# Kernel tuning notes

Hardware: AMD Instinct MI355X
Metric: run time of the kernel (lower is better)

## Reference

```python
import jax, jax.numpy as jnp
import numpy as np

B = 32
D_MODEL = 512
D_INNER = 2048
N_HEAD = 8
D_K = 64
D_V = 64


def layer_norm(x, g, b, eps=1e-5):
    m = jnp.mean(x, axis=-1, keepdims=True)
    v = jnp.mean((x - m) ** 2, axis=-1, keepdims=True)
    return (x - m) / jnp.sqrt(v + eps) * g + b


def _build_ragged():
    rs = np.random.RandomState(0)
    num_objs = rs.randint(120, 161, size=B)
    num_edges = rs.randint(480, 641, size=B)
    Lq = int(num_objs.max())
    Lv = int(num_edges.max())
    # non_pad_mask: True for valid query (entity) slots
    non_pad = np.arange(Lq)[None, :] < num_objs[:, None]  # (B, Lq)
    # slf_attn_mask semantics: True = masked out (-inf).
    # start all True, un-mask padded query rows (they get zeroed later anyway),
    # then un-mask (entity, edge) positions for each relation pair.
    mask = np.ones((B, Lq, Lv), dtype=bool)
    mask &= non_pad[:, :, None]  # pad query rows -> all False (unmasked)
    for i in range(B):
        ne, no = int(num_edges[i]), int(num_objs[i])
        j = np.arange(ne)
        subj = j % no              # guarantees every entity has >=1 edge
        obj = (j * 7 + 3) % no
        mask[i, subj, j] = False
        mask[i, obj, j] = False
    gather_idx = np.nonzero(non_pad.reshape(-1))[0].astype(np.int32)
    return Lq, Lv, non_pad, mask, gather_idx


def setup_inputs() -> dict:
    key = jax.random.key(0)
    ks = jax.random.split(key, 12)
    Lq, Lv, non_pad, mask, gather_idx = _build_ragged()
    s = 0.02
    f32 = jnp.float32
    return {
        "entity_feat": jax.random.normal(ks[0], (B, Lq, D_MODEL), f32),
        "predicate_feat": jax.random.normal(ks[1], (B, Lv, D_MODEL), f32),
        "w_qs": s * jax.random.normal(ks[2], (N_HEAD * D_K, D_MODEL), f32),
        "b_qs": jnp.zeros((N_HEAD * D_K,), f32),
        "w_ks": s * jax.random.normal(ks[3], (N_HEAD * D_K, D_MODEL), f32),
        "b_ks": jnp.zeros((N_HEAD * D_K,), f32),
        "w_vs": s * jax.random.normal(ks[4], (N_HEAD * D_V, D_MODEL), f32),
        "b_vs": jnp.zeros((N_HEAD * D_V,), f32),
        "w_fc": s * jax.random.normal(ks[5], (D_MODEL, N_HEAD * D_V), f32),
        "b_fc": jnp.zeros((D_MODEL,), f32),
        "ln1_g": jnp.ones((D_MODEL,), f32),
        "ln1_b": jnp.zeros((D_MODEL,), f32),
        "w1": s * jax.random.normal(ks[6], (D_INNER, D_MODEL), f32),
        "b1": jnp.zeros((D_INNER,), f32),
        "w2": s * jax.random.normal(ks[7], (D_MODEL, D_INNER), f32),
        "b2": jnp.zeros((D_MODEL,), f32),
        "ln2_g": jnp.ones((D_MODEL,), f32),
        "ln2_b": jnp.zeros((D_MODEL,), f32),
        "attn_mask": jnp.asarray(mask),
        "non_pad_mask": jnp.asarray(non_pad),
        "gather_idx": jnp.asarray(gather_idx),
    }


def reference(entity_feat, predicate_feat, w_qs, b_qs, w_ks, b_ks, w_vs, b_vs,
              w_fc, b_fc, ln1_g, ln1_b, w1, b1, w2, b2, ln2_g, ln2_b,
              attn_mask, non_pad_mask, gather_idx):
    Bsz, Lq, D = entity_feat.shape
    Lv = predicate_feat.shape[1]
    # multi-head cross attention: entities (queries) attend to predicates (kv)
    q = (entity_feat @ w_qs.T + b_qs).reshape(Bsz, Lq, N_HEAD, D_K)
    k = (predicate_feat @ w_ks.T + b_ks).reshape(Bsz, Lv, N_HEAD, D_K)
    v = (predicate_feat @ w_vs.T + b_vs).reshape(Bsz, Lv, N_HEAD, D_V)
    scores = jnp.einsum('bqhd,bkhd->bhqk', q, k) / jnp.sqrt(jnp.float32(D_K))
    scores = jnp.where(attn_mask[:, None, :, :], -jnp.inf, scores)
    attn = jax.nn.softmax(scores, axis=-1)
    ctx = jnp.einsum('bhqk,bkhd->bqhd', attn, v).reshape(Bsz, Lq, N_HEAD * D_V)
    out = ctx @ w_fc.T + b_fc
    out = layer_norm(out + entity_feat, ln1_g, ln1_b)
    npm = non_pad_mask[:, :, None].astype(out.dtype)
    out = out * npm
    # position-wise FFN (two 1x1 convs == linears) with residual + LayerNorm
    h = jax.nn.relu(out @ w1.T + b1)
    f = h @ w2.T + b2
    f = layer_norm(f + out, ln2_g, ln2_b)
    f = f * npm
    # unpad: gather valid entity rows
    return jnp.take(f.reshape(Bsz * Lq, D), gather_idx, axis=0)
```

## Files before the change

kernel.cpp:

```cpp
#include <hip/hip_runtime.h>
#include <math.h>

#define B_  32
#define H_  8
#define DM_ 512
#define DI_ 2048

typedef unsigned short u16;
typedef short s16x8 __attribute__((ext_vector_type(8)));
typedef short s16x4 __attribute__((ext_vector_type(4)));
typedef float f32x4 __attribute__((ext_vector_type(4)));

__device__ __forceinline__ float b2f(u16 u) {
  return __uint_as_float(((unsigned)u) << 16);
}
__device__ __forceinline__ u16 f2b(float f) {
  unsigned u = __float_as_uint(f);
  return (u16)((u + 0x7fffu + ((u >> 16) & 1u)) >> 16);
}

template<int ADT, int EPI, int RDT, int OUTF>
__global__ __launch_bounds__(256)
void gemm_mfma(const void* __restrict__ Av, const float* __restrict__ W,
               const float* __restrict__ bias, const void* __restrict__ Rv,
               void* __restrict__ Cout, int M, int N, int K)
{
  __shared__ u16 As[128 * 72];
  __shared__ u16 Bs[128 * 72];
  const int t = threadIdx.x;
  const int bm = blockIdx.y * 128, bn = blockIdx.x * 128;
  const int lane = t & 63, wave = t >> 6;
  const int lr = lane & 15, kg = lane >> 4;
  const int wr = wave >> 1, wc = wave & 1;
  const int srow = t >> 3, schk = (t & 7) * 8;

  f32x4 acc[4][4] = {};

  for (int k0 = 0; k0 < K; k0 += 64) {
#pragma unroll
    for (int p = 0; p < 4; p++) {
      const int r = srow + p * 32;
      s16x8 av = {};
      if (bm + r < M) {
        if (ADT == 0) {
          const float* ap = (const float*)Av + (size_t)(bm + r) * K + k0 + schk;
          const float4 a0 = *(const float4*)ap;
          const float4 a1 = *(const float4*)(ap + 4);
          av[0] = (short)f2b(a0.x); av[1] = (short)f2b(a0.y);
          av[2] = (short)f2b(a0.z); av[3] = (short)f2b(a0.w);
          av[4] = (short)f2b(a1.x); av[5] = (short)f2b(a1.y);
          av[6] = (short)f2b(a1.z); av[7] = (short)f2b(a1.w);
        } else {
          av = *(const s16x8*)((const u16*)Av + (size_t)(bm + r) * K + k0 + schk);
        }
      }
      *(s16x8*)&As[r * 72 + schk] = av;
      const float* wp = W + (size_t)(bn + r) * K + k0 + schk;
      const float4 w0 = *(const float4*)wp;
      const float4 w1 = *(const float4*)(wp + 4);
      s16x8 wv;
      wv[0] = (short)f2b(w0.x); wv[1] = (short)f2b(w0.y);
      wv[2] = (short)f2b(w0.z); wv[3] = (short)f2b(w0.w);
      wv[4] = (short)f2b(w1.x); wv[5] = (short)f2b(w1.y);
      wv[6] = (short)f2b(w1.z); wv[7] = (short)f2b(w1.w);
      *(s16x8*)&Bs[r * 72 + schk] = wv;
    }
    __syncthreads();
#pragma unroll
    for (int ks = 0; ks < 2; ks++) {
      s16x8 af[4], bg[4];
#pragma unroll
      for (int m = 0; m < 4; m++)
        af[m] = *(const s16x8*)&As[(wr * 64 + m * 16 + lr) * 72 + ks * 32 + kg * 8];
#pragma unroll
      for (int n = 0; n < 4; n++)
        bg[n] = *(const s16x8*)&Bs[(wc * 64 + n * 16 + lr) * 72 + ks * 32 + kg * 8];
#pragma unroll
      for (int m = 0; m < 4; m++)
#pragma unroll
        for (int n = 0; n < 4; n++)
          acc[m][n] = __builtin_amdgcn_mfma_f32_16x16x32_bf16(af[m], bg[n], acc[m][n], 0, 0, 0);
    }
    __syncthreads();
  }

  float bv[4];
#pragma unroll
  for (int n = 0; n < 4; n++) bv[n] = bias[bn + wc * 64 + n * 16 + lr];
#pragma unroll
  for (int m = 0; m < 4; m++) {
#pragma unroll
    for (int j = 0; j < 4; j++) {
      const int row = bm + wr * 64 + m * 16 + kg * 4 + j;
      if (row >= M) continue;
#pragma unroll
      for (int n = 0; n < 4; n++) {
        const int col = bn + wc * 64 + n * 16 + lr;
        float x = acc[m][n][j] + bv[n];
        if (EPI == 1) x = fmaxf(x, 0.f);
        if (EPI == 2) {
          if (RDT == 0) x += ((const float*)Rv)[(size_t)row * N + col];
          else          x += b2f(((const u16*)Rv)[(size_t)row * N + col]);
        }
        if (OUTF) ((u16*)Cout)[(size_t)row * N + col] = f2b(x);
        else      ((float*)Cout)[(size_t)row * N + col] = x;
      }
    }
  }
}

__global__ __launch_bounds__(256)
void transpose_k(const u16* __restrict__ X, u16* __restrict__ Y, int Lv, int Lvp)
{
  __shared__ u16 s[32][34];
  const int b = blockIdx.z, n0 = blockIdx.y * 32, j0 = blockIdx.x * 32;
  const int tx = threadIdx.x & 31, ty = threadIdx.x >> 5;
#pragma unroll
  for (int yy = 0; yy < 4; yy++) {
    const int j = j0 + ty + yy * 8;
    s[ty + yy * 8][tx] = (j < Lv) ? X[((size_t)b * Lv + j) * DM_ + n0 + tx] : (u16)0;
  }
  __syncthreads();
  const int j = j0 + tx;
#pragma unroll
  for (int yy = 0; yy < 4; yy++) {
    const int n = n0 + ty + yy * 8;
    Y[((size_t)b * DM_ + n) * Lvp + j] = s[tx][ty + yy * 8];
  }
}

__global__ __launch_bounds__(256)
void attn_mfma(const u16* __restrict__ Q, const u16* __restrict__ K,
               const u16* __restrict__ Vt, const int* __restrict__ mask,
               u16* __restrict__ ctxb, int Lq, int Lv, int Lvp)
{
  __shared__ u16 Ks[64][72];
  __shared__ u16 Vts[64][72];
  __shared__ u16 Plds[4][16][72];
  const float SENT = -1e30f;
  const int qb = blockIdx.x, h = blockIdx.y, b = blockIdx.z;
  const int t = threadIdx.x, w = t >> 6, lane = t & 63;
  const int lr = lane & 15, g = lane >> 4;
  const int q0 = qb * 64 + w * 16;
  const int myq = min(q0 + lr, Lq - 1);

  s16x8 qf[2];
  const u16* qptr = Q + ((size_t)b * Lq + myq) * DM_ + h * 64;
#pragma unroll
  for (int ks = 0; ks < 2; ks++) qf[ks] = *(const s16x8*)(qptr + ks * 32 + g * 8);

  const int* mrow = mask + ((size_t)b * Lq + myq) * (size_t)Lv;

  f32x4 Ot[4] = {};
  float mx = SENT, l = 0.f;

  const int srow = t >> 2, sc16 = (t & 3) * 16;
  const u16* kbase  = K + (size_t)b * Lv * DM_ + h * 64;
  const u16* vtbase = Vt + ((size_t)b * DM_ + h * 64) * (size_t)Lvp;

  for (int j0 = 0; j0 < Lv; j0 += 64) {
    __syncthreads();
    {
      const int j = j0 + srow;
      if (j < Lv) {
        const u16* kp = kbase + (size_t)j * DM_ + sc16;
        *(s16x8*)&Ks[srow][sc16]     = *(const s16x8*)kp;
        *(s16x8*)&Ks[srow][sc16 + 8] = *(const s16x8*)(kp + 8);
      } else {
        const s16x8 z = {};
        *(s16x8*)&Ks[srow][sc16] = z; *(s16x8*)&Ks[srow][sc16 + 8] = z;
      }
      const u16* vp = vtbase + (size_t)srow * Lvp + j0 + sc16;
      *(s16x8*)&Vts[srow][sc16]     = *(const s16x8*)vp;
      *(s16x8*)&Vts[srow][sc16 + 8] = *(const s16x8*)(vp + 8);
    }
    __syncthreads();

    f32x4 Sa[4] = {};
#pragma unroll
    for (int ks = 0; ks < 2; ks++) {
#pragma unroll
      for (int m = 0; m < 4; m++) {
        const s16x8 kf = *(const s16x8*)&Ks[m * 16 + lr][ks * 32 + g * 8];
        Sa[m] = __builtin_amdgcn_mfma_f32_16x16x32_bf16(kf, qf[ks], Sa[m], 0, 0, 0);
      }
    }

    float sv[4][4];
    float pm = SENT;
#pragma unroll
    for (int m = 0; m < 4; m++)
#pragma unroll
      for (int r = 0; r < 4; r++) {
        const int j = j0 + m * 16 + g * 4 + r;
        const int jc = min(j, Lv - 1);
        float x = Sa[m][r] * 0.125f;
        x = ((j >= Lv) || (mrow[jc] != 0)) ? SENT : x;
        sv[m][r] = x;
        pm = fmaxf(pm, x);
      }
    pm = fmaxf(pm, __shfl_xor(pm, 16));
    pm = fmaxf(pm, __shfl_xor(pm, 32));
    float pr[4][4];
    if (pm > -1e29f) {
      const float mn = fmaxf(mx, pm);
      const float scale = __expf(mx - mn);
      float ls = 0.f;
#pragma unroll
      for (int m = 0; m < 4; m++)
#pragma unroll
        for (int r = 0; r < 4; r++) {
          const float p = __expf(sv[m][r] - mn);
          pr[m][r] = p; ls += p;
        }
      ls += __shfl_xor(ls, 16);
      ls += __shfl_xor(ls, 32);
      l = l * scale + ls;
      mx = mn;
#pragma unroll
      for (int m = 0; m < 4; m++) Ot[m] *= scale;
    } else {
#pragma unroll
      for (int m = 0; m < 4; m++)
#pragma unroll
        for (int r = 0; r < 4; r++) pr[m][r] = 0.f;
    }

#pragma unroll
    for (int m = 0; m < 4; m++) {
      const unsigned lo = (unsigned)f2b(pr[m][0]) | ((unsigned)f2b(pr[m][1]) << 16);
      const unsigned hi = (unsigned)f2b(pr[m][2]) | ((unsigned)f2b(pr[m][3]) << 16);
      *(uint2*)&Plds[w][lr][m * 16 + g * 4] = make_uint2(lo, hi);
    }
    __syncthreads();

#pragma unroll
    for (int ks = 0; ks < 2; ks++) {
#pragma unroll
      for (int m = 0; m < 4; m++) {
        const s16x8 vf = *(const s16x8*)&Vts[m * 16 + lr][ks * 32 + g * 8];
        const s16x8 pf = *(const s16x8*)&Plds[w][lr][ks * 32 + g * 8];
        Ot[m] = __builtin_amdgcn_mfma_f32_16x16x32_bf16(vf, pf, Ot[m], 0, 0, 0);
      }
    }
  }

  __syncthreads();
  const float inv = l > 0.f ? 1.f / l : 0.f;
#pragma unroll
  for (int m = 0; m < 4; m++) {
    const unsigned lo = (unsigned)f2b(Ot[m][0] * inv) | ((unsigned)f2b(Ot[m][1] * inv) << 16);
    const unsigned hi = (unsigned)f2b(Ot[m][2] * inv) | ((unsigned)f2b(Ot[m][3] * inv) << 16);
    *(uint2*)&Plds[w][lr][m * 16 + g * 4] = make_uint2(lo, hi);
  }
  __syncthreads();
  const int oq = lane >> 2, od = (lane & 3) * 16;
  if (q0 + oq < Lq) {
    u16* op = ctxb + ((size_t)b * Lq + q0 + oq) * DM_ + h * 64 + od;
    *(s16x8*)op       = *(const s16x8*)&Plds[w][oq][od];
    *(s16x8*)(op + 8) = *(const s16x8*)&Plds[w][oq][od + 8];
  }
}

template<int OUTF>
__global__ __launch_bounds__(256)
void ln_mask_kernel(const float* __restrict__ X, const float* __restrict__ g,
                    const float* __restrict__ bta, const int* __restrict__ npm,
                    void* __restrict__ Y)
{
  __shared__ float sm[8];
  const int row = blockIdx.x;
  const int t = threadIdx.x;
  const float2 x = *(const float2*)&X[(size_t)row * DM_ + t * 2];

  float s = x.x + x.y;
#pragma unroll
  for (int o = 32; o; o >>= 1) s += __shfl_xor(s, o);
  if ((t & 63) == 0) sm[t >> 6] = s;
  __syncthreads();
  const float mean = (sm[0] + sm[1] + sm[2] + sm[3]) * (1.f / DM_);

  const float d0 = x.x - mean, d1 = x.y - mean;
  float vs = d0 * d0 + d1 * d1;
#pragma unroll
  for (int o = 32; o; o >>= 1) vs += __shfl_xor(vs, o);
  if ((t & 63) == 0) sm[4 + (t >> 6)] = vs;
  __syncthreads();
  const float var = (sm[4] + sm[5] + sm[6] + sm[7]) * (1.f / DM_);

  const float inv = rsqrtf(var + 1e-5f);
  const float np = npm[row] ? 1.f : 0.f;
  const int c = t * 2;
  const float y0 = (d0 * inv * g[c]     + bta[c])     * np;
  const float y1 = (d1 * inv * g[c + 1] + bta[c + 1]) * np;
  if (OUTF) {
    const unsigned pair = (unsigned)f2b(y0) | ((unsigned)f2b(y1) << 16);
    *(unsigned*)((u16*)Y + (size_t)row * DM_ + c) = pair;
  } else {
    *(float2*)((float*)Y + (size_t)row * DM_ + c) = make_float2(y0, y1);
  }
}

__global__ __launch_bounds__(128)
void gather_kernel(const float* __restrict__ F, const int* __restrict__ idx,
                   float* __restrict__ out)
{
  const int i = blockIdx.x;
  const int t = threadIdx.x;
  const int r = idx[i];
  *(float4*)&out[(size_t)i * DM_ + t * 4] =
      *(const float4*)&F[(size_t)r * DM_ + t * 4];
}

extern "C" void kernel_launch(void* const* d_in, const int* in_sizes, int n_in,
                              void* d_out, int out_size, void* d_ws, size_t ws_size,
                              hipStream_t stream)
{
  const float* entity = (const float*)d_in[0];
  const float* pred   = (const float*)d_in[1];
  const float* w_qs = (const float*)d_in[2];
  const float* b_qs = (const float*)d_in[3];
  const float* w_ks = (const float*)d_in[4];
  const float* b_ks = (const float*)d_in[5];
  const float* w_vs = (const float*)d_in[6];
  const float* b_vs = (const float*)d_in[7];
  const float* w_fc = (const float*)d_in[8];
  const float* b_fc = (const float*)d_in[9];
  const float* ln1g = (const float*)d_in[10];
  const float* ln1b = (const float*)d_in[11];
  const float* w1   = (const float*)d_in[12];
  const float* b1   = (const float*)d_in[13];
  const float* w2   = (const float*)d_in[14];
  const float* b2   = (const float*)d_in[15];
  const float* ln2g = (const float*)d_in[16];
  const float* ln2b = (const float*)d_in[17];
  const int* amask = (const int*)d_in[18];
  const int* npm   = (const int*)d_in[19];
  const int* gidx  = (const int*)d_in[20];

  const int Lq = in_sizes[0] / (B_ * DM_);
  const int Lv = in_sizes[1] / (B_ * DM_);
  const int Lvp = (Lv + 63) & ~63;
  const int nValid = in_sizes[20];
  const int Mq = B_ * Lq, Mv = B_ * Lv;

  auto algn = [](size_t x) { return (x + 255) & ~(size_t)255; };
  const size_t bKV  = (size_t)Mv * DM_ * 2;
  const size_t bVT  = (size_t)B_ * DM_ * Lvp * 2;
  const size_t bTMP = (size_t)Mq * DM_ * 4;
  const size_t bH   = (size_t)Mq * DI_ * 2;
  const size_t bQ   = (size_t)Mq * DM_ * 2;
  const size_t szR1 = algn(bKV > bTMP ? bKV : bTMP);
  const size_t szR2 = algn(bKV > bH ? bKV : bH);
  const size_t szR3 = algn(bQ);
  const size_t szR4 = algn(bQ);
  const size_t szR5 = algn(bVT);
  if (szR1 + szR2 + szR3 + szR4 + szR5 > ws_size) return;

  char* base = (char*)d_ws;
  char* R1 = base;
  char* R2 = R1 + szR1;
  char* R3 = R2 + szR2;
  char* R4 = R3 + szR3;
  char* R5 = R4 + szR4;

  u16*   Kb   = (u16*)R1;  float* tmp1 = (float*)R1;
  float* tmp2 = (float*)R1; float* ffin = (float*)R1;
  u16*   Vb   = (u16*)R2;  u16* hb = (u16*)R2;
  u16*   Qb   = (u16*)R3;  u16* out1 = (u16*)R3;
  u16*   ctxb = (u16*)R4;
  u16*   Vtb  = (u16*)R5;

  const dim3 blk(256);
  gemm_mfma<0, 0, 0, 1><<<dim3(DM_ / 128, (Mq + 127) / 128), blk, 0, stream>>>(
      entity, w_qs, b_qs, nullptr, Qb, Mq, DM_, DM_);
  gemm_mfma<0, 0, 0, 1><<<dim3(DM_ / 128, (Mv + 127) / 128), blk, 0, stream>>>(
      pred, w_ks, b_ks, nullptr, Kb, Mv, DM_, DM_);
  gemm_mfma<0, 0, 0, 1><<<dim3(DM_ / 128, (Mv + 127) / 128), blk, 0, stream>>>(
      pred, w_vs, b_vs, nullptr, Vb, Mv, DM_, DM_);
  transpose_k<<<dim3(Lvp / 32, DM_ / 32, B_), blk, 0, stream>>>(Vb, Vtb, Lv, Lvp);
  attn_mfma<<<dim3((Lq + 63) / 64, H_, B_), blk, 0, stream>>>(
      Qb, Kb, Vtb, amask, ctxb, Lq, Lv, Lvp);
  gemm_mfma<1, 2, 0, 0><<<dim3(DM_ / 128, (Mq + 127) / 128), blk, 0, stream>>>(
      ctxb, w_fc, b_fc, entity, tmp1, Mq, DM_, DM_);
  ln_mask_kernel<1><<<dim3(Mq), blk, 0, stream>>>(tmp1, ln1g, ln1b, npm, out1);
  gemm_mfma<1, 1, 0, 1><<<dim3(DI_ / 128, (Mq + 127) / 128), blk, 0, stream>>>(
      out1, w1, b1, nullptr, hb, Mq, DI_, DM_);
  gemm_mfma<1, 2, 1, 0><<<dim3(DM_ / 128, (Mq + 127) / 128), blk, 0, stream>>>(
      hb, w2, b2, out1, tmp2, Mq, DM_, DI_);
  ln_mask_kernel<0><<<dim3(Mq), blk, 0, stream>>>(tmp2, ln2g, ln2b, npm, ffin);
  gather_kernel<<<dim3(nValid), dim3(128), 0, stream>>>(ffin, gidx, (float*)d_out);
}
```

Before: 512.9 us.

## Pre-convert inputs and weights to bf16 and fuse K/V projections

Adds a single batched conversion kernel that turns the entity and predicate activations and all weight matrices into bf16 before any GEMM runs, so the GEMMs load bf16 directly instead of converting fp32 in every tile load. The K and V projections are merged into one GEMM with N=1024 that writes an interleaved KV buffer, using a split bias. The V transpose and the attention kernel now read from that interleaved layout. This removes repeated fp32 loads and conversion work per tile, especially for weights that many blocks re-read, at the cost of an extra conversion pass and a reorganised workspace layout.

```diff
diff --git a/kernel.cpp b/kernel.cpp
--- a/kernel.cpp
+++ b/kernel.cpp
@@ -8,7 +8,6 @@
 
 typedef unsigned short u16;
 typedef short s16x8 __attribute__((ext_vector_type(8)));
-typedef short s16x4 __attribute__((ext_vector_type(4)));
 typedef float f32x4 __attribute__((ext_vector_type(4)));
 
 __device__ __forceinline__ float b2f(u16 u) {
@@ -19,11 +18,35 @@
   return (u16)((u + 0x7fffu + ((u >> 16) & 1u)) >> 16);
 }
 
-template<int ADT, int EPI, int RDT, int OUTF>
+struct CvtSeg { const float* src; u16* dst; unsigned n4; };
+struct CvtArgs { CvtSeg s[8]; unsigned total4; };
+
 __global__ __launch_bounds__(256)
-void gemm_mfma(const void* __restrict__ Av, const float* __restrict__ W,
-               const float* __restrict__ bias, const void* __restrict__ Rv,
-               void* __restrict__ Cout, int M, int N, int K)
+void cvt_many(CvtArgs a)
+{
+  for (unsigned i = blockIdx.x * blockDim.x + threadIdx.x; i < a.total4;
+       i += gridDim.x * blockDim.x) {
+    unsigned r = i;
+#pragma unroll
+    for (int s = 0; s < 8; s++) {
+      if (r < a.s[s].n4) {
+        const float4 v = *(const float4*)(a.s[s].src + (size_t)r * 4);
+        const unsigned lo = (unsigned)f2b(v.x) | ((unsigned)f2b(v.y) << 16);
+        const unsigned hi = (unsigned)f2b(v.z) | ((unsigned)f2b(v.w) << 16);
+        *(uint2*)(a.s[s].dst + (size_t)r * 4) = make_uint2(lo, hi);
+        break;
+      }
+      r -= a.s[s].n4;
+    }
+  }
+}
+
+template<int EPI, int RDT, int OUTF, int BIAS2>
+__global__ __launch_bounds__(256)
+void gemm_bf16(const u16* __restrict__ A, const u16* __restrict__ W,
+               const float* __restrict__ bias, const float* __restrict__ bias2,
+               const void* __restrict__ Rv, void* __restrict__ Cout,
+               int M, int N, int K)
 {
   __shared__ u16 As[128 * 72];
   __shared__ u16 Bs[128 * 72];
@@ -41,28 +64,9 @@
     for (int p = 0; p < 4; p++) {
       const int r = srow + p * 32;
       s16x8 av = {};
-      if (bm + r < M) {
-        if (ADT == 0) {
-          const float* ap = (const float*)Av + (size_t)(bm + r) * K + k0 + schk;
-          const float4 a0 = *(const float4*)ap;
-          const float4 a1 = *(const float4*)(ap + 4);
-          av[0] = (short)f2b(a0.x); av[1] = (short)f2b(a0.y);
-          av[2] = (short)f2b(a0.z); av[3] = (short)f2b(a0.w);
-          av[4] = (short)f2b(a1.x); av[5] = (short)f2b(a1.y);
-          av[6] = (short)f2b(a1.z); av[7] = (short)f2b(a1.w);
-        } else {
-          av = *(const s16x8*)((const u16*)Av + (size_t)(bm + r) * K + k0 + schk);
-        }
-      }
+      if (bm + r < M) av = *(const s16x8*)&A[(size_t)(bm + r) * K + k0 + schk];
       *(s16x8*)&As[r * 72 + schk] = av;
-      const float* wp = W + (size_t)(bn + r) * K + k0 + schk;
-      const float4 w0 = *(const float4*)wp;
-      const float4 w1 = *(const float4*)(wp + 4);
-      s16x8 wv;
-      wv[0] = (short)f2b(w0.x); wv[1] = (short)f2b(w0.y);
-      wv[2] = (short)f2b(w0.z); wv[3] = (short)f2b(w0.w);
-      wv[4] = (short)f2b(w1.x); wv[5] = (short)f2b(w1.y);
-      wv[6] = (short)f2b(w1.z); wv[7] = (short)f2b(w1.w);
+      const s16x8 wv = *(const s16x8*)&W[(size_t)(bn + r) * K + k0 + schk];
       *(s16x8*)&Bs[r * 72 + schk] = wv;
     }
     __syncthreads();
@@ -84,9 +88,11 @@
     __syncthreads();
   }
 
+  const float* bp = bias;
+  if (BIAS2) bp = (bn < (N >> 1)) ? bias : (bias2 - (N >> 1));
   float bv[4];
 #pragma unroll
-  for (int n = 0; n < 4; n++) bv[n] = bias[bn + wc * 64 + n * 16 + lr];
+  for (int n = 0; n < 4; n++) bv[n] = bp[bn + wc * 64 + n * 16 + lr];
 #pragma unroll
   for (int m = 0; m < 4; m++) {
 #pragma unroll
@@ -110,7 +116,7 @@
 }
 
 __global__ __launch_bounds__(256)
-void transpose_k(const u16* __restrict__ X, u16* __restrict__ Y, int Lv, int Lvp)
+void transpose_v(const u16* __restrict__ X, u16* __restrict__ Y, int Lv, int Lvp)
 {
   __shared__ u16 s[32][34];
   const int b = blockIdx.z, n0 = blockIdx.y * 32, j0 = blockIdx.x * 32;
@@ -118,7 +124,8 @@
 #pragma unroll
   for (int yy = 0; yy < 4; yy++) {
     const int j = j0 + ty + yy * 8;
-    s[ty + yy * 8][tx] = (j < Lv) ? X[((size_t)b * Lv + j) * DM_ + n0 + tx] : (u16)0;
+    s[ty + yy * 8][tx] =
+        (j < Lv) ? X[((size_t)b * Lv + j) * 1024 + 512 + n0 + tx] : (u16)0;
   }
   __syncthreads();
   const int j = j0 + tx;
@@ -130,7 +137,7 @@
 }
 
 __global__ __launch_bounds__(256)
-void attn_mfma(const u16* __restrict__ Q, const u16* __restrict__ K,
+void attn_mfma(const u16* __restrict__ Q, const u16* __restrict__ KV,
                const u16* __restrict__ Vt, const int* __restrict__ mask,
                u16* __restrict__ ctxb, int Lq, int Lv, int Lvp)
 {
@@ -155,7 +162,7 @@
   float mx = SENT, l = 0.f;
 
   const int srow = t >> 2, sc16 = (t & 3) * 16;
-  const u16* kbase  = K + (size_t)b * Lv * DM_ + h * 64;
+  const u16* kbase  = KV + (size_t)b * Lv * 1024 + h * 64;
   const u16* vtbase = Vt + ((size_t)b * DM_ + h * 64) * (size_t)Lvp;
 
   for (int j0 = 0; j0 < Lv; j0 += 64) {
@@ -163,7 +170,7 @@
     {
       const int j = j0 + srow;
       if (j < Lv) {
-        const u16* kp = kbase + (size_t)j * DM_ + sc16;
+        const u16* kp = kbase + (size_t)j * 1024 + sc16;
         *(s16x8*)&Ks[srow][sc16]     = *(const s16x8*)kp;
         *(s16x8*)&Ks[srow][sc16 + 8] = *(const s16x8*)(kp + 8);
       } else {
@@ -345,16 +352,19 @@
   const int Mq = B_ * Lq, Mv = B_ * Lv;
 
   auto algn = [](size_t x) { return (x + 255) & ~(size_t)255; };
-  const size_t bKV  = (size_t)Mv * DM_ * 2;
-  const size_t bVT  = (size_t)B_ * DM_ * Lvp * 2;
-  const size_t bTMP = (size_t)Mq * DM_ * 4;
-  const size_t bH   = (size_t)Mq * DI_ * 2;
-  const size_t bQ   = (size_t)Mq * DM_ * 2;
-  const size_t szR1 = algn(bKV > bTMP ? bKV : bTMP);
-  const size_t szR2 = algn(bKV > bH ? bKV : bH);
-  const size_t szR3 = algn(bQ);
+  const size_t bKV   = (size_t)Mv * 1024 * 2;
+  const size_t bPred = (size_t)Mv * DM_ * 2;
+  const size_t bVT   = (size_t)B_ * DM_ * Lvp * 2;
+  const size_t bTMP  = (size_t)Mq * DM_ * 4;
+  const size_t bH    = (size_t)Mq * DI_ * 2;
+  const size_t bQ    = (size_t)Mq * DM_ * 2;
+  const size_t bW    = (size_t)(512 * 512 * 4 + 2048 * 512 * 2) * 2;
+
+  const size_t szR1 = algn(bKV > algn(bTMP) + bH ? bKV : algn(bTMP) + bH);
+  const size_t szR2 = algn(bPred > bVT ? bPred : bVT);
+  const size_t szR3 = algn(bW);
   const size_t szR4 = algn(bQ);
-  const size_t szR5 = algn(bVT);
+  const size_t szR5 = algn(bQ);
   if (szR1 + szR2 + szR3 + szR4 + szR5 > ws_size) return;
 
   char* base = (char*)d_ws;
@@ -364,30 +374,53 @@
   char* R4 = R3 + szR3;
   char* R5 = R4 + szR4;
 
-  u16*   Kb   = (u16*)R1;  float* tmp1 = (float*)R1;
-  float* tmp2 = (float*)R1; float* ffin = (float*)R1;
-  u16*   Vb   = (u16*)R2;  u16* hb = (u16*)R2;
-  u16*   Qb   = (u16*)R3;  u16* out1 = (u16*)R3;
+  u16*   KVb  = (u16*)R1;
+  float* tmp1 = (float*)R1;
+  u16*   hb   = (u16*)(R1 + algn(bTMP));
+  float* tmp2 = (float*)R1;
+  float* ffin = tmp2;
+  u16*   predB = (u16*)R2;
+  u16*   Vtb   = (u16*)R2;
+  u16*   WB   = (u16*)R3;
+  u16*   entB = (u16*)R4;
   u16*   ctxb = (u16*)R4;
-  u16*   Vtb  = (u16*)R5;
+  u16*   Qb   = (u16*)R5;
+  u16*   out1 = (u16*)R5;
+
+  u16* WQ  = WB;
+  u16* WKV = WB + 262144;
+  u16* WFC = WB + 786432;
+  u16* W1  = WB + 1048576;
+  u16* W2  = WB + 2097152;
+
+  CvtArgs ca;
+  ca.s[0] = { entity, entB,          (unsigned)(Mq * DM_ / 4) };
+  ca.s[1] = { pred,   predB,         (unsigned)(Mv * DM_ / 4) };
+  ca.s[2] = { w_qs,   WQ,            262144 / 4 };
+  ca.s[3] = { w_ks,   WKV,           262144 / 4 };
+  ca.s[4] = { w_vs,   WKV + 262144,  262144 / 4 };
+  ca.s[5] = { w_fc,   WFC,           262144 / 4 };
+  ca.s[6] = { w1,     W1,            1048576 / 4 };
+  ca.s[7] = { w2,     W2,            1048576 / 4 };
+  ca.total4 = 0;
+  for (int s = 0; s < 8; s++) ca.total4 += ca.s[s].n4;
+  cvt_many<<<dim3(2048), dim3(256), 0, stream>>>(ca);
 
   const dim3 blk(256);
-  gemm_mfma<0, 0, 0, 1><<<dim3(DM_ / 128, (Mq + 127) / 128), blk, 0, stream>>>(
-      entity, w_qs, b_qs, nullptr, Qb, Mq, DM_, DM_);
-  gemm_mfma<0, 0, 0, 1><<<dim3(DM_ / 128, (Mv + 127) / 128), blk, 0, stream>>>(
-      pred, w_ks, b_ks, nullptr, Kb, Mv, DM_, DM_);
-  gemm_mfma<0, 0, 0, 1><<<dim3(DM_ / 128, (Mv + 127) / 128), blk, 0, stream>>>(
-      pred, w_vs, b_vs, nullptr, Vb, Mv, DM_, DM_);
-  transpose_k<<<dim3(Lvp / 32, DM_ / 32, B_), blk, 0, stream>>>(Vb, Vtb, Lv, Lvp);
+  gemm_bf16<0, 0, 1, 0><<<dim3(DM_ / 128, (Mq + 127) / 128), blk, 0, stream>>>(
+      entB, WQ, b_qs, nullptr, nullptr, Qb, Mq, DM_, DM_);
+  gemm_bf16<0, 0, 1, 1><<<dim3(1024 / 128, (Mv + 127) / 128), blk, 0, stream>>>(
+      predB, WKV, b_ks, b_vs, nullptr, KVb, Mv, 1024, DM_);
+  transpose_v<<<dim3(Lvp / 32, DM_ / 32, B_), blk, 0, stream>>>(KVb, Vtb, Lv, Lvp);
   attn_mfma<<<dim3((Lq + 63) / 64, H_, B_), blk, 0, stream>>>(
-      Qb, Kb, Vtb, amask, ctxb, Lq, Lv, Lvp);
-  gemm_mfma<1, 2, 0, 0><<<dim3(DM_ / 128, (Mq + 127) / 128), blk, 0, stream>>>(
-      ctxb, w_fc, b_fc, entity, tmp1, Mq, DM_, DM_);
+      Qb, KVb, Vtb, amask, ctxb, Lq, Lv, Lvp);
+  gemm_bf16<2, 0, 0, 0><<<dim3(DM_ / 128, (Mq + 127) / 128), blk, 0, stream>>>(
+      ctxb, WFC, b_fc, nullptr, entity, tmp1, Mq, DM_, DM_);
   ln_mask_kernel<1><<<dim3(Mq), blk, 0, stream>>>(tmp1, ln1g, ln1b, npm, out1);
-  gemm_mfma<1, 1, 0, 1><<<dim3(DI_ / 128, (Mq + 127) / 128), blk, 0, stream>>>(
-      out1, w1, b1, nullptr, hb, Mq, DI_, DM_);
-  gemm_mfma<1, 2, 1, 0><<<dim3(DM_ / 128, (Mq + 127) / 128), blk, 0, stream>>>(
-      hb, w2, b2, out1, tmp2, Mq, DM_, DI_);
+  gemm_bf16<1, 0, 1, 0><<<dim3(DI_ / 128, (Mq + 127) / 128), blk, 0, stream>>>(
+      out1, W1, b1, nullptr, nullptr, hb, Mq, DI_, DM_);
+  gemm_bf16<2, 1, 0, 0><<<dim3(DM_ / 128, (Mq + 127) / 128), blk, 0, stream>>>(
+      hb, W2, b2, nullptr, out1, tmp2, Mq, DM_, DI_);
   ln_mask_kernel<0><<<dim3(Mq), blk, 0, stream>>>(tmp2, ln2g, ln2b, npm, ffin);
   gather_kernel<<<dim3(nValid), dim3(128), 0, stream>>>(ffin, gidx, (float*)d_out);
 }
```

Measured after the change: 440.7 us. 1.16x faster.
